# Optimization experiments

Measured on AMD Instinct MI355X. Metric: run time of the kernel, lower is better.

The kernel has to match this reference:

```python
import jax, jax.numpy as jnp
from jax import lax
import numpy as np

MAXDISP = 48
KSIZE = 5
DILATION = 2


def _im2col(z, k, dil):
    # z: [N,1,H,W] -> patches [N, k*k, H, W], same H,W via symmetric padding
    pad = dil * (k - 1) // 2
    return lax.conv_general_dilated_patches(
        z,
        filter_shape=(k, k),
        window_strides=(1, 1),
        padding=[(pad, pad), (pad, pad)],
        rhs_dilation=(dil, dil),
    )


def setup_inputs() -> dict:
    key = jax.random.key(0)
    k1, k2, k3, k4 = jax.random.split(key, 4)
    N, C, H, W = 2, 32, 128, 256
    x = jax.random.normal(k1, (N, C, H, W), dtype=jnp.float32)
    y = jax.random.normal(k2, (N, C, H, W), dtype=jnp.float32)
    filters = jax.random.normal(k3, (N, KSIZE * KSIZE, H, W), dtype=jnp.float32)
    filters_biases = jax.random.normal(k4, (N, 1, H, W), dtype=jnp.float32)
    return {"x": x, "y": y, "filters": filters, "filters_biases": filters_biases}


def reference(x, y, filters, filters_biases):
    N, C, H, W = x.shape
    D = MAXDISP
    # left-pad right feature with D-1 zeros along width
    y_pad = jnp.pad(y, ((0, 0), (0, 0), (0, 0), (D - 1, 0)))
    bias = filters_biases[:, 0]  # [N,H,W]

    def step(carry, start):
        y_sl = lax.dynamic_slice_in_dim(y_pad, start, W, axis=3)  # [N,C,H,W]
        z = jnp.sum(x * y_sl, axis=1, keepdims=True)              # [N,1,H,W]
        p = _im2col(z, KSIZE, DILATION)                            # [N,k*k,H,W]
        out = jnp.sum(p * filters, axis=1) + bias                  # [N,H,W]
        return carry, out

    # disparity i uses slice start D-1-i (torch loop runs d = D-1 .. 0)
    starts = (D - 1) - jnp.arange(D)
    _, corr = lax.scan(step, None, starts)   # [D,N,H,W]
    return jnp.transpose(corr, (1, 0, 2, 3))  # [N,D,H,W]
```

## Files before the change

kernel.cpp:

```cpp
#include <hip/hip_runtime.h>

#define NB 2
#define C 32
#define H 128
#define W 256
#define D 48
#define HW (H * W)

__global__ __launch_bounds__(192) void zkern(const float* __restrict__ x,
                                             const float* __restrict__ y,
                                             float* __restrict__ z) {
    const int s    = blockIdx.x;
    const int xcd  = s & 7;
    const int slot = s >> 3;
    const int half = slot & 1;
    const int t2   = slot >> 1;
    const int hi   = t2 & 15;
    const int n    = t2 >> 4;
    const int h    = xcd * 16 + hi;

    const int tid  = threadIdx.x;
    const int q    = tid & 31;
    const int dg   = tid >> 5;
    const int d0   = dg * 8;

    __shared__ __align__(16) float ys[C][184];

    const float* xrow = x + ((size_t)(n * C) * H + h) * (size_t)W;
    const float* yrow = y + ((size_t)(n * C) * H + h) * (size_t)W;
    const int ybase = 128 * half - 48;

#pragma unroll
    for (int it = 0; it < 8; ++it) {
        const int idx = it * 192 + tid;
        if (idx < 32 * 46) {
            const int r    = idx / 46;
            const int c4   = idx % 46;
            const int yidx = ybase + 4 * c4;
            float4 v = {0.f, 0.f, 0.f, 0.f};
            if (yidx >= 0 && yidx <= W - 4)
                v = *(const float4*)(yrow + (size_t)r * HW + yidx);
            *(float4*)&ys[r][4 * c4] = v;
        }
    }
    __syncthreads();

    float acc[8][4] = {};
    const int S0 = 4 * q + 40 - d0;
    const float* xcol = xrow + 128 * half + 4 * q;

#pragma unroll
    for (int cb = 0; cb < 2; ++cb) {
        float4 xr[16];
#pragma unroll
        for (int t = 0; t < 16; ++t)
            xr[t] = *(const float4*)(xcol + (size_t)(cb * 16 + t) * HW);

#pragma unroll
        for (int t = 0; t < 16; ++t) {
            const int c = cb * 16 + t;
            const float4 w0 = *(const float4*)&ys[c][S0];
            const float4 w1 = *(const float4*)&ys[c][S0 + 4];
            const float4 w2 = *(const float4*)&ys[c][S0 + 8];
            const float win[12] = {w0.x, w0.y, w0.z, w0.w,
                                   w1.x, w1.y, w1.z, w1.w,
                                   w2.x, w2.y, w2.z, w2.w};
            const float xs[4] = {xr[t].x, xr[t].y, xr[t].z, xr[t].w};
#pragma unroll
            for (int k = 0; k < 8; ++k)
#pragma unroll
                for (int o = 0; o < 4; ++o)
                    acc[k][o] += xs[o] * win[8 + o - k];
        }
    }

    float* zp = z + (((size_t)n * D + d0) * H + h) * (size_t)W + 128 * half + 4 * q;
#pragma unroll
    for (int k = 0; k < 8; ++k) {
        float4 v;
        v.x = acc[k][0]; v.y = acc[k][1]; v.z = acc[k][2]; v.w = acc[k][3];
        *(float4*)(zp + (size_t)k * HW) = v;
    }
}

#define DCH 8
#define NCH (D / DCH)
#define FGRID 768

__global__ __launch_bounds__(256) void fkern(const float* __restrict__ z,
                                             const float* __restrict__ Ff,
                                             const float* __restrict__ B,
                                             float* __restrict__ out) {
    __shared__ __align__(16) float zs[DCH][6][264];

    const int s    = blockIdx.x;
    const int xcd  = s & 7;
    const int slot = s >> 3;
    const int ch   = slot % NCH;
    const int t2   = slot / NCH;
    const int p    = t2 & 1;
    const int pl   = (t2 >> 1) & 3;
    const int n    = t2 >> 3;
    const int h0   = xcd * 16 + 4 * pl + p;
    const int d0   = ch * DCH;

    const int tid  = threadIdx.x;
    const int q    = tid & 63;
    const int r    = (tid >> 6) & 1;
    const int g2   = tid >> 7;
    const int hrow = h0 + 2 * r;

#pragma unroll
    for (int it = 0; it < 13; ++it) {
        const int idx = it * 256 + tid;
        if (idx < 48 * 66) {
            const int r2 = idx / 66;
            const int c4 = idx % 66;
            const int dd = r2 / 6;
            const int l  = r2 % 6;
            const int hh = h0 - 4 + 2 * l;
            float4 v = {0.f, 0.f, 0.f, 0.f};
            if (c4 >= 1 && c4 <= 64 && hh >= 0 && hh < H)
                v = *(const float4*)(z + (((size_t)n * D + d0 + dd) * H + hh) * (size_t)W
                                       + 4 * c4 - 4);
            *(float4*)&zs[dd][l][4 * c4] = v;
        }
    }

    const float4 bias = *(const float4*)(B + ((size_t)n * H + hrow) * (size_t)W + 4 * q);
    float acc[4][4];
#pragma unroll
    for (int k = 0; k < 4; ++k) {
        acc[k][0] = bias.x; acc[k][1] = bias.y;
        acc[k][2] = bias.z; acc[k][3] = bias.w;
    }

    __syncthreads();

#pragma unroll
    for (int i = 0; i < 5; ++i) {
        const int l = i + r;
        float4 f[5];
#pragma unroll
        for (int jj = 0; jj < 5; ++jj)
            f[jj] = *(const float4*)(Ff + (((size_t)n * 25 + i * 5 + jj) * H + hrow) * (size_t)W
                                        + 4 * q);
        const float fs[5][4] = {
            {f[0].x, f[0].y, f[0].z, f[0].w},
            {f[1].x, f[1].y, f[1].z, f[1].w},
            {f[2].x, f[2].y, f[2].z, f[2].w},
            {f[3].x, f[3].y, f[3].z, f[3].w},
            {f[4].x, f[4].y, f[4].z, f[4].w}};

#pragma unroll
        for (int k = 0; k < 4; ++k) {
            const int dd = 4 * g2 + k;
            const float4 w0 = *(const float4*)&zs[dd][l][4 * q];
            const float4 w1 = *(const float4*)&zs[dd][l][4 * q + 4];
            const float4 w2 = *(const float4*)&zs[dd][l][4 * q + 8];
            const float win[12] = {w0.x, w0.y, w0.z, w0.w,
                                   w1.x, w1.y, w1.z, w1.w,
                                   w2.x, w2.y, w2.z, w2.w};
#pragma unroll
            for (int jj = 0; jj < 5; ++jj)
#pragma unroll
                for (int o = 0; o < 4; ++o)
                    acc[k][o] += fs[jj][o] * win[o + 2 * jj];
        }
    }

#pragma unroll
    for (int k = 0; k < 4; ++k) {
        float* op = out + (((size_t)n * D + d0 + 4 * g2 + k) * H + hrow) * (size_t)W + 4 * q;
        float4 v;
        v.x = acc[k][0]; v.y = acc[k][1]; v.z = acc[k][2]; v.w = acc[k][3];
        *(float4*)op = v;
    }
}

__global__ __launch_bounds__(256) void fused_naive(const float* __restrict__ x,
                                                   const float* __restrict__ y,
                                                   const float* __restrict__ Ff,
                                                   const float* __restrict__ B,
                                                   float* __restrict__ out) {
    const size_t idx = (size_t)blockIdx.x * 256 + threadIdx.x;
    if (idx >= (size_t)NB * D * H * W) return;
    const int w = (int)(idx % W);
    const int h = (int)((idx / W) % H);
    const int d = (int)((idx / ((size_t)W * H)) % D);
    const int n = (int)(idx / ((size_t)W * H * D));

    float acc = B[((size_t)n * H + h) * W + w];
#pragma unroll
    for (int i = 0; i < 5; ++i) {
        const int hh = h + 2 * i - 4;
        if (hh < 0 || hh >= H) continue;
#pragma unroll
        for (int j = 0; j < 5; ++j) {
            const int ww = w + 2 * j - 4;
            if (ww < 0 || ww >= W) continue;
            const int ws_ = ww - d;
            float zv = 0.f;
            if (ws_ >= 0) {
                const float* xp = x + (((size_t)n * C) * H + hh) * (size_t)W + ww;
                const float* yp = y + (((size_t)n * C) * H + hh) * (size_t)W + ws_;
                for (int c = 0; c < C; ++c)
                    zv += xp[(size_t)c * HW] * yp[(size_t)c * HW];
            }
            acc += Ff[(((size_t)n * 25 + i * 5 + j) * H + h) * (size_t)W + w] * zv;
        }
    }
    out[idx] = acc;
}

extern "C" void kernel_launch(void* const* d_in, const int* in_sizes, int n_in,
                              void* d_out, int out_size, void* d_ws, size_t ws_size,
                              hipStream_t stream) {
    const float* x = (const float*)d_in[0];
    const float* y = (const float*)d_in[1];
    const float* F = (const float*)d_in[2];
    const float* B = (const float*)d_in[3];
    float* out = (float*)d_out;

    const size_t zbytes = (size_t)NB * D * H * W * sizeof(float);

    if (ws_size >= zbytes) {
        float* z = (float*)d_ws;
        zkern<<<NB * H * 2, 192, 0, stream>>>(x, y, z);
        fkern<<<FGRID, 256, 0, stream>>>(z, F, B, out);
    } else {
        const size_t total = (size_t)NB * D * H * W;
        fused_naive<<<(int)((total + 255) / 256), 256, 0, stream>>>(x, y, F, B, out);
    }
}
```

Baseline: 26.93 us.

## Fuse correlation and filter kernels into one launch with grid-wide atomic barrier

Merges the two-kernel pipeline (z correlation, then dilated 5x5 filtering) into a single persistent kernel of 512 blocks that synchronise through an atomic counter barrier in the workspace. The filter phase is retiled to 12 disparities per block so the grid matches 512 blocks, with a shared-memory union reused between phases. This removes one kernel launch and its gap but adds a memset, a spin barrier that assumes all 512 blocks are co-resident (launch_bounds 256,2), and a larger shared tile that may lower occupancy.

```diff
diff --git a/kernel.cpp b/kernel.cpp
--- a/kernel.cpp
+++ b/kernel.cpp
@@ -7,174 +7,193 @@
 #define D 48
 #define HW (H * W)
 
-__global__ __launch_bounds__(192) void zkern(const float* __restrict__ x,
-                                             const float* __restrict__ y,
-                                             float* __restrict__ z) {
-    const int s    = blockIdx.x;
-    const int xcd  = s & 7;
-    const int slot = s >> 3;
-    const int half = slot & 1;
-    const int t2   = slot >> 1;
-    const int hi   = t2 & 15;
-    const int n    = t2 >> 4;
-    const int h    = xcd * 16 + hi;
-
-    const int tid  = threadIdx.x;
-    const int q    = tid & 31;
-    const int dg   = tid >> 5;
-    const int d0   = dg * 8;
-
-    __shared__ __align__(16) float ys[C][184];
-
-    const float* xrow = x + ((size_t)(n * C) * H + h) * (size_t)W;
-    const float* yrow = y + ((size_t)(n * C) * H + h) * (size_t)W;
-    const int ybase = 128 * half - 48;
-
-#pragma unroll
-    for (int it = 0; it < 8; ++it) {
-        const int idx = it * 192 + tid;
-        if (idx < 32 * 46) {
-            const int r    = idx / 46;
-            const int c4   = idx % 46;
-            const int yidx = ybase + 4 * c4;
-            float4 v = {0.f, 0.f, 0.f, 0.f};
-            if (yidx >= 0 && yidx <= W - 4)
-                v = *(const float4*)(yrow + (size_t)r * HW + yidx);
-            *(float4*)&ys[r][4 * c4] = v;
-        }
-    }
+#define GRID 512
+#define NBLK 512u
+
+#define DCH 12
+#define NCH (D / DCH)
+
+__global__ __launch_bounds__(256, 2) void fused_kern(const float* __restrict__ x,
+                                                     const float* __restrict__ y,
+                                                     const float* __restrict__ Ff,
+                                                     const float* __restrict__ B,
+                                                     float* __restrict__ out,
+                                                     float* __restrict__ z,
+                                                     unsigned int* __restrict__ cnt) {
+    __shared__ __align__(16) union {
+        float ys[C][184];
+        float zs[DCH][6][264];
+    } sm;
+
+    const int bid = blockIdx.x;
+    const int tid = threadIdx.x;
+    const int xcd = bid & 7;
+
+    if (tid < 192) {
+        const int slot = bid >> 3;
+        const int half = slot & 1;
+        const int t2   = slot >> 1;
+        const int hi   = t2 & 15;
+        const int n    = t2 >> 4;
+        const int h    = xcd * 16 + hi;
+
+        const int q    = tid & 31;
+        const int dg   = tid >> 5;
+        const int d0   = dg * 8;
+
+        const float* xrow = x + ((size_t)(n * C) * H + h) * (size_t)W;
+        const float* yrow = y + ((size_t)(n * C) * H + h) * (size_t)W;
+        const int ybase = 128 * half - 48;
+
+#pragma unroll
+        for (int it = 0; it < 8; ++it) {
+            const int idx = it * 192 + tid;
+            if (idx < 32 * 46) {
+                const int r    = idx / 46;
+                const int c4   = idx % 46;
+                const int yidx = ybase + 4 * c4;
+                float4 v = {0.f, 0.f, 0.f, 0.f};
+                if (yidx >= 0 && yidx <= W - 4)
+                    v = *(const float4*)(yrow + (size_t)r * HW + yidx);
+                *(float4*)&sm.ys[r][4 * c4] = v;
+            }
+        }
+        __syncthreads();
+
+        float acc[8][4] = {};
+        const int S0 = 4 * q + 40 - d0;
+        const float* xcol = xrow + 128 * half + 4 * q;
+
+#pragma unroll
+        for (int cb = 0; cb < 2; ++cb) {
+            float4 xr[16];
+#pragma unroll
+            for (int t = 0; t < 16; ++t)
+                xr[t] = *(const float4*)(xcol + (size_t)(cb * 16 + t) * HW);
+
+#pragma unroll
+            for (int t = 0; t < 16; ++t) {
+                const int c = cb * 16 + t;
+                const float4 w0 = *(const float4*)&sm.ys[c][S0];
+                const float4 w1 = *(const float4*)&sm.ys[c][S0 + 4];
+                const float4 w2 = *(const float4*)&sm.ys[c][S0 + 8];
+                const float win[12] = {w0.x, w0.y, w0.z, w0.w,
+                                       w1.x, w1.y, w1.z, w1.w,
+                                       w2.x, w2.y, w2.z, w2.w};
+                const float xs[4] = {xr[t].x, xr[t].y, xr[t].z, xr[t].w};
+#pragma unroll
+                for (int k = 0; k < 8; ++k)
+#pragma unroll
+                    for (int o = 0; o < 4; ++o)
+                        acc[k][o] += xs[o] * win[8 + o - k];
+            }
+        }
+
+        float* zp = z + (((size_t)n * D + d0) * H + h) * (size_t)W + 128 * half + 4 * q;
+#pragma unroll
+        for (int k = 0; k < 8; ++k) {
+            float4 v;
+            v.x = acc[k][0]; v.y = acc[k][1]; v.z = acc[k][2]; v.w = acc[k][3];
+            *(float4*)(zp + (size_t)k * HW) = v;
+        }
+    } else {
+        __syncthreads();
+    }
+
     __syncthreads();
-
-    float acc[8][4] = {};
-    const int S0 = 4 * q + 40 - d0;
-    const float* xcol = xrow + 128 * half + 4 * q;
-
-#pragma unroll
-    for (int cb = 0; cb < 2; ++cb) {
-        float4 xr[16];
-#pragma unroll
-        for (int t = 0; t < 16; ++t)
-            xr[t] = *(const float4*)(xcol + (size_t)(cb * 16 + t) * HW);
-
-#pragma unroll
-        for (int t = 0; t < 16; ++t) {
-            const int c = cb * 16 + t;
-            const float4 w0 = *(const float4*)&ys[c][S0];
-            const float4 w1 = *(const float4*)&ys[c][S0 + 4];
-            const float4 w2 = *(const float4*)&ys[c][S0 + 8];
-            const float win[12] = {w0.x, w0.y, w0.z, w0.w,
-                                   w1.x, w1.y, w1.z, w1.w,
-                                   w2.x, w2.y, w2.z, w2.w};
-            const float xs[4] = {xr[t].x, xr[t].y, xr[t].z, xr[t].w};
-#pragma unroll
-            for (int k = 0; k < 8; ++k)
-#pragma unroll
-                for (int o = 0; o < 4; ++o)
-                    acc[k][o] += xs[o] * win[8 + o - k];
-        }
-    }
-
-    float* zp = z + (((size_t)n * D + d0) * H + h) * (size_t)W + 128 * half + 4 * q;
-#pragma unroll
-    for (int k = 0; k < 8; ++k) {
-        float4 v;
-        v.x = acc[k][0]; v.y = acc[k][1]; v.z = acc[k][2]; v.w = acc[k][3];
-        *(float4*)(zp + (size_t)k * HW) = v;
-    }
-}
-
-#define DCH 8
-#define NCH (D / DCH)
-#define FGRID 768
-
-__global__ __launch_bounds__(256) void fkern(const float* __restrict__ z,
-                                             const float* __restrict__ Ff,
-                                             const float* __restrict__ B,
-                                             float* __restrict__ out) {
-    __shared__ __align__(16) float zs[DCH][6][264];
-
-    const int s    = blockIdx.x;
-    const int xcd  = s & 7;
-    const int slot = s >> 3;
-    const int ch   = slot % NCH;
-    const int t2   = slot / NCH;
-    const int p    = t2 & 1;
-    const int pl   = (t2 >> 1) & 3;
-    const int n    = t2 >> 3;
-    const int h0   = xcd * 16 + 4 * pl + p;
-    const int d0   = ch * DCH;
-
-    const int tid  = threadIdx.x;
-    const int q    = tid & 63;
-    const int r    = (tid >> 6) & 1;
-    const int g2   = tid >> 7;
-    const int hrow = h0 + 2 * r;
-
-#pragma unroll
-    for (int it = 0; it < 13; ++it) {
-        const int idx = it * 256 + tid;
-        if (idx < 48 * 66) {
-            const int r2 = idx / 66;
-            const int c4 = idx % 66;
-            const int dd = r2 / 6;
-            const int l  = r2 % 6;
-            const int hh = h0 - 4 + 2 * l;
-            float4 v = {0.f, 0.f, 0.f, 0.f};
-            if (c4 >= 1 && c4 <= 64 && hh >= 0 && hh < H)
-                v = *(const float4*)(z + (((size_t)n * D + d0 + dd) * H + hh) * (size_t)W
-                                       + 4 * c4 - 4);
-            *(float4*)&zs[dd][l][4 * c4] = v;
-        }
-    }
-
-    const float4 bias = *(const float4*)(B + ((size_t)n * H + hrow) * (size_t)W + 4 * q);
-    float acc[4][4];
-#pragma unroll
-    for (int k = 0; k < 4; ++k) {
-        acc[k][0] = bias.x; acc[k][1] = bias.y;
-        acc[k][2] = bias.z; acc[k][3] = bias.w;
-    }
-
+    if (tid == 0) {
+        __builtin_amdgcn_fence(__ATOMIC_RELEASE, "agent");
+        __hip_atomic_fetch_add(cnt, 1u, __ATOMIC_RELAXED, __HIP_MEMORY_SCOPE_AGENT);
+        unsigned int v = 0;
+        long guard = 0;
+        do {
+            v = __hip_atomic_load(cnt, __ATOMIC_RELAXED, __HIP_MEMORY_SCOPE_AGENT);
+        } while (v < NBLK && ++guard < 2000000);
+    }
     __syncthreads();
-
-#pragma unroll
-    for (int i = 0; i < 5; ++i) {
-        const int l = i + r;
-        float4 f[5];
-#pragma unroll
-        for (int jj = 0; jj < 5; ++jj)
-            f[jj] = *(const float4*)(Ff + (((size_t)n * 25 + i * 5 + jj) * H + hrow) * (size_t)W
-                                        + 4 * q);
-        const float fs[5][4] = {
-            {f[0].x, f[0].y, f[0].z, f[0].w},
-            {f[1].x, f[1].y, f[1].z, f[1].w},
-            {f[2].x, f[2].y, f[2].z, f[2].w},
-            {f[3].x, f[3].y, f[3].z, f[3].w},
-            {f[4].x, f[4].y, f[4].z, f[4].w}};
-
-#pragma unroll
-        for (int k = 0; k < 4; ++k) {
-            const int dd = 4 * g2 + k;
-            const float4 w0 = *(const float4*)&zs[dd][l][4 * q];
-            const float4 w1 = *(const float4*)&zs[dd][l][4 * q + 4];
-            const float4 w2 = *(const float4*)&zs[dd][l][4 * q + 8];
-            const float win[12] = {w0.x, w0.y, w0.z, w0.w,
-                                   w1.x, w1.y, w1.z, w1.w,
-                                   w2.x, w2.y, w2.z, w2.w};
+    __builtin_amdgcn_fence(__ATOMIC_ACQUIRE, "agent");
+
+    {
+        const int slot = bid >> 3;
+        const int ch   = slot & 3;
+        const int t2   = slot >> 2;
+        const int p    = t2 & 1;
+        const int pl   = (t2 >> 1) & 3;
+        const int n    = t2 >> 3;
+        const int h0   = xcd * 16 + 4 * pl + p;
+        const int d0   = ch * DCH;
+
+        const int q    = tid & 63;
+        const int r    = (tid >> 6) & 1;
+        const int g2   = tid >> 7;
+        const int hrow = h0 + 2 * r;
+
+#pragma unroll
+        for (int it = 0; it < 19; ++it) {
+            const int idx = it * 256 + tid;
+            if (idx < 72 * 66) {
+                const int r2 = idx / 66;
+                const int c4 = idx % 66;
+                const int dd = r2 / 6;
+                const int l  = r2 % 6;
+                const int hh = h0 - 4 + 2 * l;
+                float4 v = {0.f, 0.f, 0.f, 0.f};
+                if (c4 >= 1 && c4 <= 64 && hh >= 0 && hh < H)
+                    v = *(const float4*)(z + (((size_t)n * D + d0 + dd) * H + hh) * (size_t)W
+                                           + 4 * c4 - 4);
+                *(float4*)&sm.zs[dd][l][4 * c4] = v;
+            }
+        }
+
+        const float4 bias = *(const float4*)(B + ((size_t)n * H + hrow) * (size_t)W + 4 * q);
+        float acc[6][4];
+#pragma unroll
+        for (int k = 0; k < 6; ++k) {
+            acc[k][0] = bias.x; acc[k][1] = bias.y;
+            acc[k][2] = bias.z; acc[k][3] = bias.w;
+        }
+
+        __syncthreads();
+
+#pragma unroll
+        for (int i = 0; i < 5; ++i) {
+            const int l = i + r;
+            float4 f[5];
 #pragma unroll
             for (int jj = 0; jj < 5; ++jj)
-#pragma unroll
-                for (int o = 0; o < 4; ++o)
-                    acc[k][o] += fs[jj][o] * win[o + 2 * jj];
-        }
-    }
-
-#pragma unroll
-    for (int k = 0; k < 4; ++k) {
-        float* op = out + (((size_t)n * D + d0 + 4 * g2 + k) * H + hrow) * (size_t)W + 4 * q;
-        float4 v;
-        v.x = acc[k][0]; v.y = acc[k][1]; v.z = acc[k][2]; v.w = acc[k][3];
-        *(float4*)op = v;
+                f[jj] = *(const float4*)(Ff + (((size_t)n * 25 + i * 5 + jj) * H + hrow)
+                                               * (size_t)W + 4 * q);
+            const float fs[5][4] = {
+                {f[0].x, f[0].y, f[0].z, f[0].w},
+                {f[1].x, f[1].y, f[1].z, f[1].w},
+                {f[2].x, f[2].y, f[2].z, f[2].w},
+                {f[3].x, f[3].y, f[3].z, f[3].w},
+                {f[4].x, f[4].y, f[4].z, f[4].w}};
+
+#pragma unroll
+            for (int k = 0; k < 6; ++k) {
+                const int dd = 6 * g2 + k;
+                const float4 w0 = *(const float4*)&sm.zs[dd][l][4 * q];
+                const float4 w1 = *(const float4*)&sm.zs[dd][l][4 * q + 4];
+                const float4 w2 = *(const float4*)&sm.zs[dd][l][4 * q + 8];
+                const float win[12] = {w0.x, w0.y, w0.z, w0.w,
+                                       w1.x, w1.y, w1.z, w1.w,
+                                       w2.x, w2.y, w2.z, w2.w};
+#pragma unroll
+                for (int jj = 0; jj < 5; ++jj)
+#pragma unroll
+                    for (int o = 0; o < 4; ++o)
+                        acc[k][o] += fs[jj][o] * win[o + 2 * jj];
+            }
+        }
+
+#pragma unroll
+        for (int k = 0; k < 6; ++k) {
+            float* op = out + (((size_t)n * D + d0 + 6 * g2 + k) * H + hrow) * (size_t)W + 4 * q;
+            float4 v;
+            v.x = acc[k][0]; v.y = acc[k][1]; v.z = acc[k][2]; v.w = acc[k][3];
+            *(float4*)op = v;
+        }
     }
 }
 
@@ -224,10 +243,11 @@
 
     const size_t zbytes = (size_t)NB * D * H * W * sizeof(float);
 
-    if (ws_size >= zbytes) {
+    if (ws_size >= zbytes + 64) {
         float* z = (float*)d_ws;
-        zkern<<<NB * H * 2, 192, 0, stream>>>(x, y, z);
-        fkern<<<FGRID, 256, 0, stream>>>(z, F, B, out);
+        unsigned int* cnt = (unsigned int*)((char*)d_ws + zbytes);
+        hipMemsetAsync((void*)cnt, 0, sizeof(unsigned int), stream);
+        fused_kern<<<GRID, 256, 0, stream>>>(x, y, F, B, out, z, cnt);
     } else {
         const size_t total = (size_t)NB * D * H * W;
         fused_naive<<<(int)((total + 255) / 256), 256, 0, stream>>>(x, y, F, B, out);
```

New measurement: 91.31 us. 3.39x slower.
